# Kernel tuning notes

Measured on AMD Instinct MI355X. Metric: run time of the kernel, lower is better.

The kernel has to match this reference:

```python
import jax, jax.numpy as jnp
import numpy as np

TEMP = 0.1
EPS = 1e-12


def _l2_normalize(x):
    n = jnp.sqrt(jnp.sum(x * x, axis=1, keepdims=True))
    return x / jnp.maximum(n, EPS)


def _unif(x, t=2.0):
    # log-mean of exp(-t * squared pairwise distances), over unordered pairs (torch.pdist)
    g = x @ x.T                       # [n, n] gram
    sq = jnp.diagonal(g)
    d2 = jnp.maximum(sq[:, None] + sq[None, :] - 2.0 * g, 0.0)
    n = x.shape[0]
    iu = jnp.triu(jnp.ones((n, n), dtype=bool), k=1)
    s = jnp.where(iu, jnp.exp(-t * d2), 0.0).sum()
    return jnp.log(s / (n * (n - 1) / 2))


def setup_inputs() -> dict:
    key = jax.random.key(0)
    k1, k2 = jax.random.split(key)
    B, D = 4096, 1024
    return {
        "proj_1": jax.random.normal(k1, (B, D), dtype=jnp.float32),
        "proj_2": jax.random.normal(k2, (B, D), dtype=jnp.float32),
    }


def reference(proj_1, proj_2):
    B = proj_1.shape[0]
    z_i = _l2_normalize(proj_1)
    z_j = _l2_normalize(proj_2)
    z = jnp.concatenate([z_i, z_j], axis=0)          # [2B, D]
    # cosine similarity of unit vectors == dot product (normalize + GEMM)
    sim = z @ z.T                                     # [2B, 2B]

    idx = jnp.arange(B)
    sim_ij = sim[idx, idx + B]                        # diag(sim, +B)
    sim_ji = sim[idx + B, idx]                        # diag(sim, -B)
    positives = jnp.concatenate([sim_ij, sim_ji], axis=0)  # [2B]

    mask = ~jnp.eye(2 * B, dtype=bool)
    denom = jnp.where(mask, jnp.exp(sim / TEMP), 0.0).sum(axis=1)  # [2B]
    all_losses = -(positives / TEMP - jnp.log(denom))
    loss = all_losses.sum() / (2 * B)

    lalign = jax.lax.stop_gradient(
        jnp.mean(jnp.sum((z_i - z_j) ** 2, axis=1))   # ||.||_2^alpha with alpha=2
    )
    half = B // 2
    lunif = jax.lax.stop_gradient(
        (_unif(z_i[:half]) + _unif(z_i[half:])) / 2.0
    )
    return loss, lalign, lunif
```

## Files before the change

kernel.cpp:

```cpp
#include <hip/hip_runtime.h>
#include <hip/hip_bf16.h>
#include <math.h>

#define DIM 1024
#define NB  4096
#define N2  8192
#define BT  256
#define NT2 32
#define PS  34
#define GRID_FULL 512
#define GRID_ALL  576

typedef int i32x4 __attribute__((ext_vector_type(4)));

__device__ __forceinline__ void gload_lds16(const unsigned char* g, unsigned char* l) {
    __builtin_amdgcn_global_load_lds((__attribute__((address_space(1))) void*)(g),
                                     (__attribute__((address_space(3))) void*)(l),
                                     16, 0, 0);
}

__device__ __forceinline__ unsigned int pk4_i8(float a, float b, float c, float d) {
    const int ia = __float2int_rn(a * 127.0f), ib = __float2int_rn(b * 127.0f);
    const int ic = __float2int_rn(c * 127.0f), id = __float2int_rn(d * 127.0f);
    return (unsigned)(ia & 255) | ((unsigned)(ib & 255) << 8) |
           ((unsigned)(ic & 255) << 16) | ((unsigned)(id & 255) << 24);
}

__global__ __launch_bounds__(256) void norm_kernel(
    const float* __restrict__ p1, const float* __restrict__ p2,
    unsigned char* __restrict__ zq, float* __restrict__ pos)
{
    const int r = blockIdx.x;
    const int t = threadIdx.x;
    const float4 x1 = ((const float4*)(p1 + (size_t)r * DIM))[t];
    const float4 x2 = ((const float4*)(p2 + (size_t)r * DIM))[t];
    float s1  = x1.x*x1.x + x1.y*x1.y + x1.z*x1.z + x1.w*x1.w;
    float s2  = x2.x*x2.x + x2.y*x2.y + x2.z*x2.z + x2.w*x2.w;
    float s12 = x1.x*x2.x + x1.y*x2.y + x1.z*x2.z + x1.w*x2.w;
#pragma unroll
    for (int off = 1; off < 64; off <<= 1) {
        s1  += __shfl_xor(s1,  off);
        s2  += __shfl_xor(s2,  off);
        s12 += __shfl_xor(s12, off);
    }
    __shared__ float ls[3][4];
    const int wid = t >> 6;
    if ((t & 63) == 0) { ls[0][wid] = s1; ls[1][wid] = s2; ls[2][wid] = s12; }
    __syncthreads();
    s1  = ls[0][0] + ls[0][1] + ls[0][2] + ls[0][3];
    s2  = ls[1][0] + ls[1][1] + ls[1][2] + ls[1][3];
    s12 = ls[2][0] + ls[2][1] + ls[2][2] + ls[2][3];
    const float rn1 = 1.0f / fmaxf(sqrtf(s1), 1e-12f);
    const float rn2 = 1.0f / fmaxf(sqrtf(s2), 1e-12f);
    if (t == 0) pos[r] = s12 * rn1 * rn2;

    const int j0 = (t << 2) & 63;
    const int kb = t >> 4;
    const int pb = (j0 < 32) ? (((j0 >> 3) << 4) + (j0 & 7))
                             : ((((j0 - 32) >> 3) << 4) + 8 + ((j0 - 32) & 7));
    const size_t off8 = (size_t)kb * 64 + pb;
    *(unsigned int*)(zq + (size_t)r * DIM + off8) =
        pk4_i8(x1.x * rn1, x1.y * rn1, x1.z * rn1, x1.w * rn1);
    *(unsigned int*)(zq + (size_t)(NB + r) * DIM + off8) =
        pk4_i8(x2.x * rn2, x2.y * rn2, x2.z * rn2, x2.w * rn2);
}

__global__ __launch_bounds__(1024, 4) void sim_kernel(
    const unsigned char* __restrict__ zq,
    float* __restrict__ partials,
    float* __restrict__ lup)
{
    __shared__ __align__(16) unsigned char buf[2][2][BT * 64];
    const int t    = threadIdx.x;
    const int lane = t & 63;
    const int wid  = t >> 6;
    const int fr   = lane & 15;
    const int kg   = lane >> 4;
    const int cb   = ((kg ^ ((fr >> 1) & 3)) << 4);
    const int srow_l = lane >> 2;
    const int sgr  = (((lane & 3) ^ ((lane >> 3) & 3)) << 4);
    const int rsub = (lane >> 4) << 2;
    const int csub = lane & 15;
    const float inv = 1.0f / 16129.0f;
    const int bid = blockIdx.x;

    if (bid < GRID_FULL) {
        int jj = (bid & 7) * 64 + (bid >> 3);
#pragma unroll 1
        for (int k = 16; k < 32; ++k) {
            const int e = k * 32 - ((k * (k - 1)) >> 1);
            if (jj >= e) ++jj;
        }
        int rt = 0;
        while ((rt + 1) * 32 - (((rt + 1) * rt) >> 1) <= jj) ++rt;
        const int ct = rt + jj - (rt * 32 - ((rt * (rt - 1)) >> 1));
        const bool isdiag = (rt == ct);
        const int row0 = rt << 8;
        const int col0 = ct << 8;
        const int wr = wid >> 2;
        const int wc = wid & 3;

        const int aoff = (((wr << 6) + fr) << 6) + cb;
        const int boff = (((wc << 6) + fr) << 6) + cb;
        const unsigned char* Ab[2] = { &buf[0][0][0] + aoff, &buf[1][0][0] + aoff };
        const unsigned char* Bb[2] = { &buf[0][1][0] + boff, &buf[1][1][0] + boff };

        const int srow = (wid << 4) + srow_l;
        const unsigned char* arow = zq + (size_t)(row0 + srow) * DIM + sgr;
        const unsigned char* bcol = zq + (size_t)(col0 + srow) * DIM + sgr;

        i32x4 acc[4][4] = {};
        gload_lds16(arow, &buf[0][0][wid << 10]);
        gload_lds16(bcol, &buf[0][1][wid << 10]);
        __syncthreads();

#pragma unroll
        for (int kt = 0; kt < 16; ++kt) {
            const int cur = kt & 1;
            if (kt < 15) {
                gload_lds16(arow + (kt + 1) * 64, &buf[cur ^ 1][0][wid << 10]);
                gload_lds16(bcol + (kt + 1) * 64, &buf[cur ^ 1][1][wid << 10]);
            }
            i32x4 bq[4];
#pragma unroll
            for (int n = 0; n < 4; ++n)
                bq[n] = *(const i32x4*)(Bb[cur] + (n << 10));
#pragma unroll
            for (int m = 0; m < 4; ++m) {
                const i32x4 aq = *(const i32x4*)(Ab[cur] + (m << 10));
#pragma unroll
                for (int n = 0; n < 4; ++n)
                    acc[m][n] = __builtin_amdgcn_mfma_i32_16x16x64_i8(aq, bq[n], acc[m][n], 0, 0, 0);
            }
            __syncthreads();
        }

        float* rsum4 = (float*)&buf[0][0][0];
        float* csum4 = rsum4 + 1024;
        float* lured = csum4 + 1024;
        const bool inreg = (ct < 8) || (rt >= 8 && ct < 16);
        const int  rbase = row0 + (wr << 6);
        const int  cbase = col0 + (wc << 6);

        float lu = 0.0f;
        float cs[4] = {0.0f, 0.0f, 0.0f, 0.0f};
#pragma unroll
        for (int m = 0; m < 4; ++m) {
            float rs[4] = {0.0f, 0.0f, 0.0f, 0.0f};
#pragma unroll
            for (int n = 0; n < 4; ++n) {
                const int gcol = cbase + (n << 4) + csub;
#pragma unroll
                for (int r = 0; r < 4; ++r) {
                    const int grow = rbase + (m << 4) + rsub + r;
                    const float s = (float)acc[m][n][r] * inv;
                    float e = __expf(10.0f * s);
                    if (isdiag) e = (grow != gcol) ? e : 0.0f;
                    rs[r] += e;
                    cs[n] += e;
                    if (inreg && (!isdiag || gcol > grow)) {
                        const float d2 = fmaxf(2.0f - 2.0f * s, 0.0f);
                        lu += __expf(-2.0f * d2);
                    }
                }
            }
#pragma unroll
            for (int off = 1; off < 16; off <<= 1) {
#pragma unroll
                for (int r = 0; r < 4; ++r) rs[r] += __shfl_xor(rs[r], off);
            }
            if ((lane & 15) == 0) {
#pragma unroll
                for (int r = 0; r < 4; ++r)
                    rsum4[((wr << 6) + (m << 4) + rsub + r) * 4 + wc] = rs[r];
            }
        }
        if (!isdiag) {
#pragma unroll
            for (int off = 16; off < 64; off <<= 1) {
#pragma unroll
                for (int n = 0; n < 4; ++n) cs[n] += __shfl_xor(cs[n], off);
            }
            if (lane < 16) {
#pragma unroll
                for (int n = 0; n < 4; ++n)
                    csum4[((wc << 6) + (n << 4) + lane) * 4 + wr] = cs[n];
            }
        }
#pragma unroll
        for (int off = 1; off < 64; off <<= 1) lu += __shfl_xor(lu, off);
        if (lane == 0) lured[wid] = lu;
        __syncthreads();

        if (t == 0) {
            float s = 0.0f;
#pragma unroll
            for (int w = 0; w < 16; ++w) s += lured[w];
            lup[rt * NT2 + ct] = s;
        }
        if (t < 256) {
            const float* p = rsum4 + t * 4;
            partials[(size_t)(row0 + t) * PS + ct] = ((p[0] + p[1]) + p[2]) + p[3];
        } else if (t < 512 && !isdiag) {
            const float* p = csum4 + (t - 256) * 4;
            partials[(size_t)(col0 + t - 256) * PS + rt] = ((p[0] + p[1]) + p[2]) + p[3];
        }
    } else {
        const int q  = bid - GRID_FULL;
        const int k  = 16 + (q >> 2);
        const int qr = (q >> 1) & 1;
        const int qc = q & 1;
        const int row0 = (k << 8) + (qr << 7);
        const int col0 = (k << 8) + (qc << 7);
        const int wr = wid >> 2;
        const int wc = wid & 3;

        const int chl = wid & 7;
        const int isB = wid >> 3;
        const unsigned char* spanel =
            zq + (size_t)((isB ? col0 : row0) + (chl << 4) + srow_l) * DIM + sgr;
        unsigned char* dst0 = &buf[0][isB][chl << 10];
        unsigned char* dst1 = &buf[1][isB][chl << 10];

        i32x4 acc[2][2] = {};
        gload_lds16(spanel, dst0);
        __syncthreads();

#pragma unroll
        for (int kt = 0; kt < 16; ++kt) {
            const int cur = kt & 1;
            if (kt < 15) gload_lds16(spanel + (kt + 1) * 64, cur ? dst0 : dst1);
            const unsigned char* Ab = &buf[cur][0][0];
            const unsigned char* Bb = &buf[cur][1][0];
            i32x4 aq[2], bq[2];
#pragma unroll
            for (int n = 0; n < 2; ++n)
                bq[n] = *(const i32x4*)(Bb + ((((wc << 5) + (n << 4) + fr) << 6) + cb));
#pragma unroll
            for (int m = 0; m < 2; ++m)
                aq[m] = *(const i32x4*)(Ab + ((((wr << 5) + (m << 4) + fr) << 6) + cb));
#pragma unroll
            for (int m = 0; m < 2; ++m)
#pragma unroll
                for (int n = 0; n < 2; ++n)
                    acc[m][n] = __builtin_amdgcn_mfma_i32_16x16x64_i8(aq[m], bq[n], acc[m][n], 0, 0, 0);
            __syncthreads();
        }

        float* rsum4 = (float*)&buf[0][0][0];
#pragma unroll
        for (int m = 0; m < 2; ++m) {
            float rs[4] = {0.0f, 0.0f, 0.0f, 0.0f};
#pragma unroll
            for (int n = 0; n < 2; ++n) {
                const int gcol = col0 + (wc << 5) + (n << 4) + csub;
#pragma unroll
                for (int r = 0; r < 4; ++r) {
                    const int grow = row0 + (wr << 5) + (m << 4) + rsub + r;
                    const float s = (float)acc[m][n][r] * inv;
                    float e = __expf(10.0f * s);
                    e = (grow != gcol) ? e : 0.0f;
                    rs[r] += e;
                }
            }
#pragma unroll
            for (int off = 1; off < 16; off <<= 1) {
#pragma unroll
                for (int r = 0; r < 4; ++r) rs[r] += __shfl_xor(rs[r], off);
            }
            if ((lane & 15) == 0) {
#pragma unroll
                for (int r = 0; r < 4; ++r)
                    rsum4[((wr << 5) + (m << 4) + rsub + r) * 4 + wc] = rs[r];
            }
        }
        __syncthreads();
        if (t < 128) {
            const float* p = rsum4 + t * 4;
            partials[(size_t)(row0 + t) * PS + (qc ? 32 : k)] =
                ((p[0] + p[1]) + p[2]) + p[3];
        }
    }
}

__global__ __launch_bounds__(128) void logred_kernel(
    const float* __restrict__ partials, double* __restrict__ red_log)
{
    const int t   = threadIdx.x;
    const int row = blockIdx.x * 128 + t;
    const float* p = partials + (size_t)row * PS;
    float dsum = 0.0f;
#pragma unroll
    for (int i = 0; i < 33; ++i) dsum += p[i];
    double l = log((double)dsum);
    __shared__ double sd[128];
    sd[t] = l;
    __syncthreads();
    for (int s = 64; s > 0; s >>= 1) {
        if (t < s) sd[t] += sd[t + s];
        __syncthreads();
    }
    if (t == 0) red_log[blockIdx.x] = sd[0];
}

__global__ __launch_bounds__(256) void final_kernel(
    const double* __restrict__ red_log, const float* __restrict__ pos,
    const float* __restrict__ lup, float* __restrict__ out)
{
    const int t = threadIdx.x;
    double dlog = 0.0, dpos = 0.0, ds1 = 0.0, ds2 = 0.0;
    if (t < 64) dlog = red_log[t];
    for (int i = t; i < NB; i += 256) dpos += (double)pos[i];
    for (int i = t; i < NT2 * NT2; i += 256) {
        const int rt = i >> 5, ct = i & 31;
        if (rt > ct) continue;
        const double v = (double)lup[i];
        if (rt < 8 && ct < 8) ds1 += v;
        else if (rt >= 8 && rt < 16 && ct >= 8 && ct < 16) ds2 += v;
    }
    __shared__ double sd[4][256];
    sd[0][t] = dlog; sd[1][t] = dpos; sd[2][t] = ds1; sd[3][t] = ds2;
    __syncthreads();
    for (int s = 128; s > 0; s >>= 1) {
        if (t < s) {
            sd[0][t] += sd[0][t + s]; sd[1][t] += sd[1][t + s];
            sd[2][t] += sd[2][t + s]; sd[3][t] += sd[3][t + s];
        }
        __syncthreads();
    }
    if (t == 0) {
        const double mean_pos = sd[1][0] / (double)NB;
        const double loss   = sd[0][0] / (double)N2 - mean_pos * 10.0;
        const double lalign = 2.0 - 2.0 * mean_pos;
        const double C      = 2048.0 * 2047.0 * 0.5;
        const double lunif  = 0.5 * (log(sd[2][0] / C) + log(sd[3][0] / C));
        out[0] = (float)loss;
        out[1] = (float)lalign;
        out[2] = (float)lunif;
    }
}

extern "C" void kernel_launch(void* const* d_in, const int* in_sizes, int n_in,
                              void* d_out, int out_size, void* d_ws, size_t ws_size,
                              hipStream_t stream) {
    const float* p1 = (const float*)d_in[0];
    const float* p2 = (const float*)d_in[1];
    float* out = (float*)d_out;

    char* ws = (char*)d_ws;
    unsigned char* zq = (unsigned char*)ws;
    float*  partials  = (float*)(ws + ((size_t)8 << 20));
    float*  pos       = (float*)(ws + ((size_t)10 << 20));
    float*  lup       = (float*)(ws + ((size_t)10 << 20) + 16384);
    double* red_log   = (double*)(ws + ((size_t)10 << 20) + 16384 + 4096);

    hipMemsetAsync(partials, 0, (size_t)N2 * PS * sizeof(float), stream);
    hipLaunchKernelGGL(norm_kernel,   dim3(NB),       dim3(256),  0, stream, p1, p2, zq, pos);
    hipLaunchKernelGGL(sim_kernel,    dim3(GRID_ALL), dim3(1024), 0, stream, zq, partials, lup);
    hipLaunchKernelGGL(logred_kernel, dim3(64),       dim3(128),  0, stream, partials, red_log);
    hipLaunchKernelGGL(final_kernel,  dim3(1),        dim3(256),  0, stream, red_log, pos, lup, out);
}
```

Baseline: 81.72 us.

## Double K-step per stage to halve barriers and fold exp scaling constants

Raises the K chunk per pipeline stage from 64 to 128 bytes, doubling the LDS buffers and using a new 8-way XOR swizzle. This halves the number of __syncthreads and load stages in both the full-tile and diagonal-quadrant paths. It also folds the int8 dequant scale, temperature and log2e into single exp2f constants so the epilogue drops several multiplies. The cost is twice the LDS use, which may reduce occupancy under launch_bounds(1024,4).

```diff
diff --git a/kernel.cpp b/kernel.cpp
--- a/kernel.cpp
+++ b/kernel.cpp
@@ -10,6 +10,10 @@
 #define PS  34
 #define GRID_FULL 512
 #define GRID_ALL  576
+
+#define C1f 8.9447146e-4f
+#define C2f 3.5778876e-4f
+#define C2b (-5.7707802f)
 
 typedef int i32x4 __attribute__((ext_vector_type(4)));
 
@@ -70,18 +74,16 @@
     float* __restrict__ partials,
     float* __restrict__ lup)
 {
-    __shared__ __align__(16) unsigned char buf[2][2][BT * 64];
+    __shared__ __align__(16) unsigned char buf[2][2][BT * 128];
     const int t    = threadIdx.x;
     const int lane = t & 63;
     const int wid  = t >> 6;
     const int fr   = lane & 15;
     const int kg   = lane >> 4;
-    const int cb   = ((kg ^ ((fr >> 1) & 3)) << 4);
-    const int srow_l = lane >> 2;
-    const int sgr  = (((lane & 3) ^ ((lane >> 3) & 3)) << 4);
+    const int cb0  = ((kg ^ (fr & 7)) << 4);
+    const int sgr8 = (((lane & 7) ^ ((lane >> 3) & 7)) << 4);
     const int rsub = (lane >> 4) << 2;
     const int csub = lane & 15;
-    const float inv = 1.0f / 16129.0f;
     const int bid = blockIdx.x;
 
     if (bid < GRID_FULL) {
@@ -100,40 +102,49 @@
         const int wr = wid >> 2;
         const int wc = wid & 3;
 
-        const int aoff = (((wr << 6) + fr) << 6) + cb;
-        const int boff = (((wc << 6) + fr) << 6) + cb;
-        const unsigned char* Ab[2] = { &buf[0][0][0] + aoff, &buf[1][0][0] + aoff };
-        const unsigned char* Bb[2] = { &buf[0][1][0] + boff, &buf[1][1][0] + boff };
-
-        const int srow = (wid << 4) + srow_l;
-        const unsigned char* arow = zq + (size_t)(row0 + srow) * DIM + sgr;
-        const unsigned char* bcol = zq + (size_t)(col0 + srow) * DIM + sgr;
+        const int abase = ((wr << 6) + fr) << 7;
+        const int bbase = ((wc << 6) + fr) << 7;
+
+        const int ar0 = row0 + ((wid << 1) << 3) + (lane >> 3);
+        const int br0 = col0 + ((wid << 1) << 3) + (lane >> 3);
+        const unsigned char* asrc = zq + (size_t)ar0 * DIM + sgr8;
+        const unsigned char* bsrc = zq + (size_t)br0 * DIM + sgr8;
+
+#define STAGEF(bsel, kp) do { \
+        gload_lds16(asrc + (kp) * 128,              &buf[bsel][0][(wid << 11)]); \
+        gload_lds16(asrc + (size_t)8 * DIM + (kp) * 128, &buf[bsel][0][(wid << 11) + 1024]); \
+        gload_lds16(bsrc + (kp) * 128,              &buf[bsel][1][(wid << 11)]); \
+        gload_lds16(bsrc + (size_t)8 * DIM + (kp) * 128, &buf[bsel][1][(wid << 11) + 1024]); \
+    } while (0)
 
         i32x4 acc[4][4] = {};
-        gload_lds16(arow, &buf[0][0][wid << 10]);
-        gload_lds16(bcol, &buf[0][1][wid << 10]);
-        __syncthreads();
-
-#pragma unroll
-        for (int kt = 0; kt < 16; ++kt) {
-            const int cur = kt & 1;
-            if (kt < 15) {
-                gload_lds16(arow + (kt + 1) * 64, &buf[cur ^ 1][0][wid << 10]);
-                gload_lds16(bcol + (kt + 1) * 64, &buf[cur ^ 1][1][wid << 10]);
-            }
-            i32x4 bq[4];
-#pragma unroll
-            for (int n = 0; n < 4; ++n)
-                bq[n] = *(const i32x4*)(Bb[cur] + (n << 10));
-#pragma unroll
-            for (int m = 0; m < 4; ++m) {
-                const i32x4 aq = *(const i32x4*)(Ab[cur] + (m << 10));
+        STAGEF(0, 0);
+        __syncthreads();
+
+#pragma unroll
+        for (int kp = 0; kp < 8; ++kp) {
+            const int cur = kp & 1;
+            if (kp < 7) STAGEF(cur ^ 1, kp + 1);
+            const unsigned char* Ab = &buf[cur][0][0] + abase;
+            const unsigned char* Bb = &buf[cur][1][0] + bbase;
+#pragma unroll
+            for (int h = 0; h < 2; ++h) {
+                const int cbh = cb0 ^ (h << 6);
+                i32x4 bq[4];
 #pragma unroll
                 for (int n = 0; n < 4; ++n)
-                    acc[m][n] = __builtin_amdgcn_mfma_i32_16x16x64_i8(aq, bq[n], acc[m][n], 0, 0, 0);
+                    bq[n] = *(const i32x4*)(Bb + (n << 11) + cbh);
+#pragma unroll
+                for (int m = 0; m < 4; ++m) {
+                    const i32x4 aq = *(const i32x4*)(Ab + (m << 11) + cbh);
+#pragma unroll
+                    for (int n = 0; n < 4; ++n)
+                        acc[m][n] = __builtin_amdgcn_mfma_i32_16x16x64_i8(aq, bq[n], acc[m][n], 0, 0, 0);
+                }
             }
             __syncthreads();
         }
+#undef STAGEF
 
         float* rsum4 = (float*)&buf[0][0][0];
         float* csum4 = rsum4 + 1024;
@@ -153,15 +164,13 @@
 #pragma unroll
                 for (int r = 0; r < 4; ++r) {
                     const int grow = rbase + (m << 4) + rsub + r;
-                    const float s = (float)acc[m][n][r] * inv;
-                    float e = __expf(10.0f * s);
+                    const float f = (float)acc[m][n][r];
+                    float e = exp2f(f * C1f);
                     if (isdiag) e = (grow != gcol) ? e : 0.0f;
                     rs[r] += e;
                     cs[n] += e;
-                    if (inreg && (!isdiag || gcol > grow)) {
-                        const float d2 = fmaxf(2.0f - 2.0f * s, 0.0f);
-                        lu += __expf(-2.0f * d2);
-                    }
+                    if (inreg && (!isdiag || gcol > grow))
+                        lu += exp2f(fmaf(f, C2f, C2b));
                 }
             }
 #pragma unroll
@@ -215,35 +224,45 @@
         const int wr = wid >> 2;
         const int wc = wid & 3;
 
-        const int chl = wid & 7;
-        const int isB = wid >> 3;
+        const int ch  = wid << 1;
+        const int isB = ch >> 4;
+        const int chl = ch & 15;
         const unsigned char* spanel =
-            zq + (size_t)((isB ? col0 : row0) + (chl << 4) + srow_l) * DIM + sgr;
-        unsigned char* dst0 = &buf[0][isB][chl << 10];
-        unsigned char* dst1 = &buf[1][isB][chl << 10];
+            zq + (size_t)((isB ? col0 : row0) + (chl << 3) + (lane >> 3)) * DIM + sgr8;
+        unsigned char* d0a = &buf[0][isB][chl << 10];
+        unsigned char* d1a = &buf[1][isB][chl << 10];
 
         i32x4 acc[2][2] = {};
-        gload_lds16(spanel, dst0);
-        __syncthreads();
-
-#pragma unroll
-        for (int kt = 0; kt < 16; ++kt) {
-            const int cur = kt & 1;
-            if (kt < 15) gload_lds16(spanel + (kt + 1) * 64, cur ? dst0 : dst1);
-            const unsigned char* Ab = &buf[cur][0][0];
-            const unsigned char* Bb = &buf[cur][1][0];
-            i32x4 aq[2], bq[2];
-#pragma unroll
-            for (int n = 0; n < 2; ++n)
-                bq[n] = *(const i32x4*)(Bb + ((((wc << 5) + (n << 4) + fr) << 6) + cb));
-#pragma unroll
-            for (int m = 0; m < 2; ++m)
-                aq[m] = *(const i32x4*)(Ab + ((((wr << 5) + (m << 4) + fr) << 6) + cb));
-#pragma unroll
-            for (int m = 0; m < 2; ++m)
+        gload_lds16(spanel, d0a);
+        gload_lds16(spanel + (size_t)8 * DIM, d0a + 1024);
+        __syncthreads();
+
+#pragma unroll
+        for (int kp = 0; kp < 8; ++kp) {
+            const int cur = kp & 1;
+            if (kp < 7) {
+                unsigned char* dn = cur ? d0a : d1a;
+                gload_lds16(spanel + (kp + 1) * 128, dn);
+                gload_lds16(spanel + (size_t)8 * DIM + (kp + 1) * 128, dn + 1024);
+            }
+            const unsigned char* Ab = &buf[cur][0][0] + (((wr << 5) + fr) << 7);
+            const unsigned char* Bb = &buf[cur][1][0] + (((wc << 5) + fr) << 7);
+#pragma unroll
+            for (int h = 0; h < 2; ++h) {
+                const int cbh = cb0 ^ (h << 6);
+                i32x4 aq[2], bq[2];
 #pragma unroll
                 for (int n = 0; n < 2; ++n)
-                    acc[m][n] = __builtin_amdgcn_mfma_i32_16x16x64_i8(aq[m], bq[n], acc[m][n], 0, 0, 0);
+                    bq[n] = *(const i32x4*)(Bb + (n << 11) + cbh);
+#pragma unroll
+                for (int m = 0; m < 2; ++m)
+                    aq[m] = *(const i32x4*)(Ab + (m << 11) + cbh);
+#pragma unroll
+                for (int m = 0; m < 2; ++m)
+#pragma unroll
+                    for (int n = 0; n < 2; ++n)
+                        acc[m][n] = __builtin_amdgcn_mfma_i32_16x16x64_i8(aq[m], bq[n], acc[m][n], 0, 0, 0);
+            }
             __syncthreads();
         }
 
@@ -257,8 +276,7 @@
 #pragma unroll
                 for (int r = 0; r < 4; ++r) {
                     const int grow = row0 + (wr << 5) + (m << 4) + rsub + r;
-                    const float s = (float)acc[m][n][r] * inv;
-                    float e = __expf(10.0f * s);
+                    float e = exp2f((float)acc[m][n][r] * C1f);
                     e = (grow != gcol) ? e : 0.0f;
                     rs[r] += e;
                 }
```

New measurement: 79.71 us. -2.5%, faster.
